# Optimization experiments

Measured on AMD Instinct MI355X. Metric: run time of the kernel, lower is better.

## Reference

```python
import jax, jax.numpy as jnp
import numpy as np

BLOCK_NUM = 64
B, M, K, N = 4, 4096, 4096, 4096  # batch, rows, in_features, out_features


def setup_inputs() -> dict:
    key = jax.random.key(0)
    k1, k2 = jax.random.split(key)
    x = jax.random.normal(k1, (B, M, K), dtype=jnp.float32)
    weight = jax.random.normal(k2, (K, N), dtype=jnp.float32) * 0.02
    return {"x": x, "weight": weight}


def reference(x, weight):
    # Block-local matmul: output block (i, j) = A_block(i, j) @ W_block(i, j).
    # No cross-block reduction: each (i, j) output block depends on exactly one
    # A block and one W block. Vectorized as a single einsum over all blocks.
    b, m, k = x.shape
    k2, n = weight.shape
    Bn = BLOCK_NUM
    r, c, o = m // Bn, k // Bn, n // Bn  # per-block rows / contract / cols
    A = x.reshape(b, Bn, r, Bn, c)        # [b, i, r, j, c]
    W = weight.reshape(Bn, c, Bn, o)      # [i, c, j, o] (rows split by i, cols by j)
    out = jnp.einsum('birjc,icjo->birjo', A, W)
    return out.reshape(b, m, n)
```

## Files before the change

### kernel.cpp

```cpp
#include <hip/hip_runtime.h>
#include <hip/hip_bf16.h>


typedef short bf16x8 __attribute__((ext_vector_type(8)));
typedef float f32x4 __attribute__((ext_vector_type(4)));

__device__ __forceinline__ unsigned short f2bf(float f) {
    union { float f; unsigned int u; } v; v.f = f;
    unsigned int u = v.u;
    u += 0x7fffu + ((u >> 16) & 1u);
    return (unsigned short)(u >> 16);
}

__device__ __forceinline__ unsigned long long pack4(float4 v) {
    return  (unsigned long long)f2bf(v.x)        |
           ((unsigned long long)f2bf(v.y) << 16) |
           ((unsigned long long)f2bf(v.z) << 32) |
           ((unsigned long long)f2bf(v.w) << 48);
}

__device__ __forceinline__ unsigned long long pack4s(float a, float b,
                                                     float c, float d) {
    return  (unsigned long long)f2bf(a)        |
           ((unsigned long long)f2bf(b) << 16) |
           ((unsigned long long)f2bf(c) << 32) |
           ((unsigned long long)f2bf(d) << 48);
}

#define BELEMS 16777216ull

#define FENCE() asm volatile("s_waitcnt lgkmcnt(0)" ::: "memory")

__global__ __launch_bounds__(256, 2) void block_matmul_kernel(
    const float* __restrict__ x, const float* __restrict__ w,
    float* __restrict__ out) {
    __shared__ char smem[65536];

    const int t   = threadIdx.x;
    const int l   = t & 63;
    const int wv  = t >> 6;
    const int lr  = l & 15;
    const int lhi = l >> 4;

    int orig = blockIdx.x;
    int wg   = (orig & 7) * 512 + (orig >> 3);
    int b  = wg >> 10;
    int i  = (wg >> 4) & 63;
    int q8 = wg & 15;

    const size_t rowbase = (size_t)i * 64;
    const size_t colbase = (size_t)q8 * 256;

    const float* Ab = x + (size_t)b * BELEMS + rowbase * 4096 + colbase;
    const float* Wb = w + rowbase * 4096 + colbase;
    float*       Ob = out + (size_t)b * BELEMS + rowbase * 4096 + colbase;

    float4 areg[16];
    {
        const float* p = Ab + (size_t)(wv * 16) * 4096 + l * 4;
        #pragma unroll
        for (int s = 0; s < 16; ++s)
            areg[s] = *reinterpret_cast<const float4*>(p + (size_t)s * 4096);
    }
    float wreg[16][4];
    {
        const float* p = Wb + (size_t)(wv * 16) * 4096 + l;
        #pragma unroll
        for (int s = 0; s < 16; ++s)
            #pragma unroll
            for (int h = 0; h < 4; ++h)
                wreg[s][h] = p[(size_t)s * 4096 + h * 64];
    }

    #pragma unroll
    for (int s = 0; s < 16; ++s) {
        int m = wv * 16 + s;
        *reinterpret_cast<unsigned long long*>(
            smem + m * 512 + ((l * 8) ^ ((m & 7) << 4))) = pack4(areg[s]);
    }
    #pragma unroll
    for (int g = 0; g < 4; ++g) {
        int c0 = wv * 16 + g * 4;
        #pragma unroll
        for (int h = 0; h < 4; ++h) {
            int n = l + h * 64;
            unsigned long long pk = pack4s(wreg[g*4+0][h], wreg[g*4+1][h],
                                           wreg[g*4+2][h], wreg[g*4+3][h]);
            *reinterpret_cast<unsigned long long*>(
                smem + 32768 + n * 128 + ((c0 * 2) ^ ((n & 7) << 4))) = pk;
        }
    }

    __syncthreads();

    f32x4 acc[4][4];
    #pragma unroll
    for (int a = 0; a < 4; ++a)
        #pragma unroll
        for (int z = 0; z < 4; ++z) acc[a][z] = (f32x4){0.f,0.f,0.f,0.f};

    const int m = wv * 16 + lr;
    #pragma unroll
    for (int jloc = 0; jloc < 4; ++jloc) {
        #pragma unroll
        for (int kt = 0; kt < 2; ++kt) {
            bf16x8 af = *reinterpret_cast<const bf16x8*>(
                smem + m * 512 +
                ((jloc * 128 + kt * 64 + lhi * 16) ^ ((m & 7) << 4)));
            #pragma unroll
            for (int nt = 0; nt < 4; ++nt) {
                int n = jloc * 64 + nt * 16 + lr;
                bf16x8 bfr = *reinterpret_cast<const bf16x8*>(
                    smem + 32768 + n * 128 +
                    ((kt * 64 + lhi * 16) ^ ((n & 7) << 4)));
                acc[jloc][nt] = __builtin_amdgcn_mfma_f32_16x16x32_bf16(
                    af, bfr, acc[jloc][nt], 0, 0, 0);
            }
        }
    }

    __syncthreads();

    #pragma unroll
    for (int jloc = 0; jloc < 4; ++jloc)
        #pragma unroll
        for (int nt = 0; nt < 4; ++nt)
            #pragma unroll
            for (int r = 0; r < 4; ++r) {
                int mr  = wv * 16 + lhi * 4 + r;
                int col = jloc * 64 + nt * 16 + lr;
                *reinterpret_cast<float*>(
                    smem + mr * 1024 + ((col * 4) ^ ((mr & 7) << 4)))
                    = acc[jloc][nt][r];
            }
    FENCE();

    #pragma unroll
    for (int s = 0; s < 16; ++s) {
        int mr = wv * 16 + s;
        f32x4 v = *reinterpret_cast<const f32x4*>(
            smem + mr * 1024 + ((l * 16) ^ ((mr & 7) << 4)));
        *reinterpret_cast<f32x4*>(Ob + (size_t)mr * 4096 + l * 4) = v;
    }
}

extern "C" void kernel_launch(void* const* d_in, const int* in_sizes, int n_in,
                              void* d_out, int out_size, void* d_ws, size_t ws_size,
                              hipStream_t stream) {
    const float* x = (const float*)d_in[0];
    const float* w = (const float*)d_in[1];
    float* out = (float*)d_out;

    dim3 grid(4096);
    dim3 block(256);
    block_matmul_kernel<<<grid, block, 0, stream>>>(x, w, out);
}
```

Measured before the change: 128.3 us.

## Make blocks persistent over eight column tiles with prefetched A loads

The grid shrinks from 4096 to 512 workgroups. Each workgroup now loops over 8 consecutive 256-column tiles, and the A tile for the next iteration is loaded into registers while the current MFMA work runs. Output goes straight from the accumulators to global memory with nontemporal scalar stores, replacing the LDS transpose and the vectorized write. The aim is to cut launch and tail overhead and hide load latency, at the cost of fewer waves in flight, W loads that are not prefetched, and stores that are less coalesced.

```diff
diff --git a/kernel.cpp b/kernel.cpp
--- a/kernel.cpp
+++ b/kernel.cpp
@@ -29,8 +29,6 @@
 
 #define BELEMS 16777216ull
 
-#define FENCE() asm volatile("s_waitcnt lgkmcnt(0)" ::: "memory")
-
 __global__ __launch_bounds__(256, 2) void block_matmul_kernel(
     const float* __restrict__ x, const float* __restrict__ w,
     float* __restrict__ out) {
@@ -43,104 +41,94 @@
     const int lhi = l >> 4;
 
     int orig = blockIdx.x;
-    int wg   = (orig & 7) * 512 + (orig >> 3);
-    int b  = wg >> 10;
-    int i  = (wg >> 4) & 63;
-    int q8 = wg & 15;
+    int xcd  = orig & 7;
+    int idx  = orig >> 3;
+    int i = xcd * 8 + (idx >> 3);
+    int b = (idx >> 1) & 3;
+    int h = idx & 1;
 
     const size_t rowbase = (size_t)i * 64;
-    const size_t colbase = (size_t)q8 * 256;
+    const size_t colbase = (size_t)h * 2048;
 
-    const float* Ab = x + (size_t)b * BELEMS + rowbase * 4096 + colbase;
+    const float* Ab = x + (size_t)b * BELEMS + (rowbase + wv * 16) * 4096 + colbase;
     const float* Wb = w + rowbase * 4096 + colbase;
-    float*       Ob = out + (size_t)b * BELEMS + rowbase * 4096 + colbase;
+    float*       Ob = out + (size_t)b * BELEMS + (rowbase + wv * 16) * 4096 + colbase;
 
     float4 areg[16];
-    {
-        const float* p = Ab + (size_t)(wv * 16) * 4096 + l * 4;
-        #pragma unroll
-        for (int s = 0; s < 16; ++s)
-            areg[s] = *reinterpret_cast<const float4*>(p + (size_t)s * 4096);
-    }
-    float wreg[16][4];
-    {
-        const float* p = Wb + (size_t)(wv * 16) * 4096 + l;
-        #pragma unroll
-        for (int s = 0; s < 16; ++s)
-            #pragma unroll
-            for (int h = 0; h < 4; ++h)
-                wreg[s][h] = p[(size_t)s * 4096 + h * 64];
-    }
 
-    #pragma unroll
-    for (int s = 0; s < 16; ++s) {
-        int m = wv * 16 + s;
-        *reinterpret_cast<unsigned long long*>(
-            smem + m * 512 + ((l * 8) ^ ((m & 7) << 4))) = pack4(areg[s]);
-    }
-    #pragma unroll
-    for (int g = 0; g < 4; ++g) {
-        int c0 = wv * 16 + g * 4;
-        #pragma unroll
-        for (int h = 0; h < 4; ++h) {
-            int n = l + h * 64;
-            unsigned long long pk = pack4s(wreg[g*4+0][h], wreg[g*4+1][h],
-                                           wreg[g*4+2][h], wreg[g*4+3][h]);
-            *reinterpret_cast<unsigned long long*>(
-                smem + 32768 + n * 128 + ((c0 * 2) ^ ((n & 7) << 4))) = pk;
-        }
-    }
+#define ISSUE_A(c_) { const float* p_ = Ab + (size_t)(c_) * 256 + l * 4;      \
+    _Pragma("unroll") for (int s = 0; s < 16; ++s)                            \
+        areg[s] = *reinterpret_cast<const float4*>(p_ + (size_t)s * 4096); }
 
+#define WRITE_A() { _Pragma("unroll") for (int s = 0; s < 16; ++s) {          \
+        int m_ = wv * 16 + s;                                                 \
+        *reinterpret_cast<unsigned long long*>(                               \
+            smem + m_ * 512 + ((l * 8) ^ ((m_ & 7) << 4))) = pack4(areg[s]); } }
+
+#define STAGE_W(c_) {                                                         \
+    const float* p_ = Wb + (size_t)(wv * 16) * 4096 + (size_t)(c_) * 256 + l; \
+    float wr_[16][4];                                                         \
+    _Pragma("unroll") for (int s = 0; s < 16; ++s)                            \
+        _Pragma("unroll") for (int hh = 0; hh < 4; ++hh)                      \
+            wr_[s][hh] = p_[(size_t)s * 4096 + hh * 64];                      \
+    _Pragma("unroll") for (int g = 0; g < 4; ++g)                             \
+        _Pragma("unroll") for (int hh = 0; hh < 4; ++hh) {                    \
+            int n_  = hh * 64 + l;                                            \
+            int cc_ = (wv * 16 + g * 4) * 2;                                  \
+            unsigned long long pk_ = pack4s(wr_[g*4+0][hh], wr_[g*4+1][hh],   \
+                                            wr_[g*4+2][hh], wr_[g*4+3][hh]);  \
+            *reinterpret_cast<unsigned long long*>(                           \
+                smem + 32768 + n_ * 128 + (cc_ ^ ((n_ & 7) << 4))) = pk_; } }
+
+    ISSUE_A(0);
+    WRITE_A();
+    STAGE_W(0);
     __syncthreads();
 
-    f32x4 acc[4][4];
-    #pragma unroll
-    for (int a = 0; a < 4; ++a)
+    #pragma unroll 1
+    for (int c = 0; c < 8; ++c) {
+        if (c < 7) ISSUE_A(c + 1);
+
+        f32x4 acc[4][4];
         #pragma unroll
-        for (int z = 0; z < 4; ++z) acc[a][z] = (f32x4){0.f,0.f,0.f,0.f};
+        for (int a = 0; a < 4; ++a)
+            #pragma unroll
+            for (int z = 0; z < 4; ++z) acc[a][z] = (f32x4){0.f,0.f,0.f,0.f};
 
-    const int m = wv * 16 + lr;
-    #pragma unroll
-    for (int jloc = 0; jloc < 4; ++jloc) {
+        const int m = wv * 16 + lr;
         #pragma unroll
-        for (int kt = 0; kt < 2; ++kt) {
-            bf16x8 af = *reinterpret_cast<const bf16x8*>(
-                smem + m * 512 +
-                ((jloc * 128 + kt * 64 + lhi * 16) ^ ((m & 7) << 4)));
+        for (int jloc = 0; jloc < 4; ++jloc) {
             #pragma unroll
-            for (int nt = 0; nt < 4; ++nt) {
-                int n = jloc * 64 + nt * 16 + lr;
-                bf16x8 bfr = *reinterpret_cast<const bf16x8*>(
-                    smem + 32768 + n * 128 +
-                    ((kt * 64 + lhi * 16) ^ ((n & 7) << 4)));
-                acc[jloc][nt] = __builtin_amdgcn_mfma_f32_16x16x32_bf16(
-                    af, bfr, acc[jloc][nt], 0, 0, 0);
+            for (int kt = 0; kt < 2; ++kt) {
+                bf16x8 af = *reinterpret_cast<const bf16x8*>(
+                    smem + m * 512 +
+                    ((jloc * 128 + kt * 64 + lhi * 16) ^ ((m & 7) << 4)));
+                #pragma unroll
+                for (int nt = 0; nt < 4; ++nt) {
+                    int bn = jloc * 64 + nt * 16 + lr;
+                    bf16x8 bfr = *reinterpret_cast<const bf16x8*>(
+                        smem + 32768 + bn * 128 +
+                        ((kt * 64 + lhi * 16) ^ ((bn & 7) << 4)));
+                    acc[jloc][nt] = __builtin_amdgcn_mfma_f32_16x16x32_bf16(
+                        af, bfr, acc[jloc][nt], 0, 0, 0);
+                }
             }
         }
-    }
 
-    __syncthreads();
+        float* Op = Ob + (size_t)c * 256;
+        #pragma unroll
+        for (int jloc = 0; jloc < 4; ++jloc)
+            #pragma unroll
+            for (int nt = 0; nt < 4; ++nt)
+                #pragma unroll
+                for (int r = 0; r < 4; ++r)
+                    __builtin_nontemporal_store(acc[jloc][nt][r],
+                        Op + (size_t)(lhi * 4 + r) * 4096 +
+                        jloc * 64 + nt * 16 + lr);
 
-    #pragma unroll
-    for (int jloc = 0; jloc < 4; ++jloc)
-        #pragma unroll
-        for (int nt = 0; nt < 4; ++nt)
-            #pragma unroll
-            for (int r = 0; r < 4; ++r) {
-                int mr  = wv * 16 + lhi * 4 + r;
-                int col = jloc * 64 + nt * 16 + lr;
-                *reinterpret_cast<float*>(
-                    smem + mr * 1024 + ((col * 4) ^ ((mr & 7) << 4)))
-                    = acc[jloc][nt][r];
-            }
-    FENCE();
-
-    #pragma unroll
-    for (int s = 0; s < 16; ++s) {
-        int mr = wv * 16 + s;
-        f32x4 v = *reinterpret_cast<const f32x4*>(
-            smem + mr * 1024 + ((l * 16) ^ ((mr & 7) << 4)));
-        *reinterpret_cast<f32x4*>(Ob + (size_t)mr * 4096 + l * 4) = v;
+        __syncthreads();
+        if (c < 7) { WRITE_A(); STAGE_W(c + 1); }
+        __syncthreads();
     }
 }
 
@@ -151,7 +139,7 @@
     const float* w = (const float*)d_in[1];
     float* out = (float*)d_out;
 
-    dim3 grid(4096);
+    dim3 grid(512);
     dim3 block(256);
     block_matmul_kernel<<<grid, block, 0, stream>>>(x, w, out);
 }
```

Result: slower. 197.3 us (+53.8%).
